# Performance work log

Measured on AMD Instinct MI355X. Metric: run time of the kernel, lower is better.

## Reference

```python
import jax, jax.numpy as jnp
import numpy as np

# Complete K-ary forest: B trees, depth D levels, BFS node numbering per tree.
B, K, D = 64, 4, 6
V, L = 600, 256
N_PER = (K ** D - 1) // (K - 1)   # 1365 nodes per tree
N = B * N_PER                      # 87360 total nodes


def _schedule():
    """Per-(depth, sibling_index) groups, mirroring the torch decode_train loop
    for a complete K-ary forest. Returns list of (d, s, node_idx, parent_idx)."""
    starts = [(K ** d - 1) // (K - 1) for d in range(D)]  # level offsets within a tree
    tree_off = np.arange(B)[:, None] * N_PER
    groups = []
    for d in range(D):
        for s in (range(1) if d == 0 else range(K)):
            if d == 0:
                p = np.arange(1)                      # root
                par = None
            else:
                p = np.arange(K ** (d - 1)) * K + s   # positions with sib_pos == s
                par = (tree_off + starts[d - 1] + (p // K)[None, :]).reshape(-1)
            idx = (tree_off + starts[d] + p[None, :]).reshape(-1)
            groups.append((d, s, jnp.asarray(idx),
                           None if par is None else jnp.asarray(par)))
    return groups

GROUPS = _schedule()


def _lstm(gx, h, c, W_hh, b_ih, b_hh):
    # torch LSTMCell, gate order i, f, g, o; gx = x @ W_ih^T precomputed.
    gates = gx + b_ih + h @ W_hh.T + b_hh
    i, f, g, o = jnp.split(gates, 4, axis=1)
    c_new = jax.nn.sigmoid(f) * c + jax.nn.sigmoid(i) * jnp.tanh(g)
    return jax.nn.sigmoid(o) * jnp.tanh(c_new), c_new


def setup_inputs() -> dict:
    key = jax.random.key(0)
    ks = jax.random.split(key, 20)
    w = lambda k, shape, s=0.05: jax.random.normal(k, shape, dtype=jnp.float32) * s
    return {
        'z': w(ks[0], (B, L), 1.0),
        'features': jax.random.randint(ks[1], (N,), 0, V),
        'W_ih_p': w(ks[2], (4 * L, V)), 'W_hh_p': w(ks[3], (4 * L, L)),
        'b_ih_p': w(ks[4], (4 * L,)), 'b_hh_p': w(ks[5], (4 * L,)),
        'W_ih_s': w(ks[6], (4 * L, V)), 'W_hh_s': w(ks[7], (4 * L, L)),
        'b_ih_s': w(ks[8], (4 * L,)), 'b_hh_s': w(ks[9], (4 * L,)),
        'U_parent': w(ks[10], (L, L)), 'U_sibling': w(ks[11], (L, L)),
        'W_label': w(ks[12], (V, L)), 'b_label': w(ks[13], (V,)),
        'W_depth': w(ks[14], (1, L)), 'b_depth': w(ks[15], (1,)),
        'W_width': w(ks[16], (1, L)), 'b_width': w(ks[17], (1,)),
        'w_off_p': w(ks[18], (1, 1), 1.0), 'w_off_s': w(ks[19], (1, 1), 1.0),
    }


def reference(z, features, W_ih_p, W_hh_p, b_ih_p, b_hh_p,
              W_ih_s, W_hh_s, b_ih_s, b_hh_s, U_parent, U_sibling,
              W_label, b_label, W_depth, b_depth, W_width, b_width,
              w_off_p, w_off_s):
    h_p = jnp.zeros((N, L), jnp.float32)
    c_p = jnp.zeros((N, L), jnp.float32)
    h_s = jnp.zeros((N, L), jnp.float32)
    c_s = jnp.zeros((N, L), jnp.float32)
    pred_labels = jnp.zeros((N, V), jnp.float32)
    pred_is_parent = jnp.zeros((N,), jnp.float32)
    pred_has_sib = jnp.zeros((N,), jnp.float32)

    for d, s, idx, pidx in GROUPS:
        G = idx.shape[0]
        if d == 0:
            h_par, c_par = z, jnp.zeros((B, L), jnp.float32)
        else:
            h_par, c_par = h_p[pidx], c_p[pidx]
        if s == 0:
            h_prev = jnp.zeros((G, L), jnp.float32)
            c_prev = jnp.zeros((G, L), jnp.float32)
        else:
            h_prev, c_prev = h_s[idx - 1], c_s[idx - 1]
        # group-constant teacher flags for a complete K-ary tree
        is_par = 1.0 if d < D - 1 else 0.0
        has_sib = 1.0 if (d > 0 and s < K - 1) else 0.0

        h_pred = jnp.tanh(h_par @ U_parent.T + h_prev @ U_sibling.T)
        logits = h_pred @ W_label.T + b_label
        p_par = jax.nn.sigmoid(h_pred @ W_depth.T + b_depth)[:, 0]
        p_sib = jax.nn.sigmoid(h_pred @ W_width.T + b_width)[:, 0]
        logp = jax.nn.log_softmax(
            logits + w_off_p[0, 0] * is_par + w_off_s[0, 0] * has_sib, axis=1)

        lab = features[idx]
        gx_p = jnp.take(W_ih_p, lab, axis=1).T  # one-hot @ W_ih^T as a gather
        gx_s = jnp.take(W_ih_s, lab, axis=1).T
        hp_new, cp_new = _lstm(gx_p, h_par, c_par, W_hh_p, b_ih_p, b_hh_p)
        hs_new, cs_new = _lstm(gx_s, h_prev, c_prev, W_hh_s, b_ih_s, b_hh_s)

        h_p = h_p.at[idx].set(hp_new)
        c_p = c_p.at[idx].set(cp_new)
        h_s = h_s.at[idx].set(hs_new)
        c_s = c_s.at[idx].set(cs_new)
        pred_labels = pred_labels.at[idx].set(logp)
        pred_is_parent = pred_is_parent.at[idx].set(p_par)
        pred_has_sib = pred_has_sib.at[idx].set(p_sib)

    # pack [N, V+2]: log-softmax labels, p(is_parent), p(has_sibling)
    return jnp.concatenate(
        [pred_labels, pred_is_parent[:, None], pred_has_sib[:, None]], axis=1)
```

## Files before the change

### kernel.cpp

```cpp
#include <hip/hip_runtime.h>


typedef unsigned short u16;
typedef short bf16x8 __attribute__((ext_vector_type(8)));
typedef float f32x4 __attribute__((ext_vector_type(4)));

#define NPER 1365
#define VDIM 600
#define VD2  602

#define MODE_PPA   0
#define MODE_UPROJ 1
#define MODE_ROOT  2

__device__ __forceinline__ float b2f(u16 h) {
  union { unsigned u; float f; } v; v.u = ((unsigned)h) << 16; return v.f;
}
__device__ __forceinline__ u16 f2bf(float f) {
  union { float f; unsigned u; } v; v.f = f;
  unsigned r = v.u + 0x7fff + ((v.u >> 16) & 1);
  return (u16)(r >> 16);
}
__device__ __forceinline__ float fsigm(float x) {
  return __fdividef(1.f, 1.f + __expf(-x));
}
__device__ __forceinline__ float ftanh(float x) {
  float e = __expf(-2.f * fabsf(x));
  float r = __fdividef(1.f - e, 1.f + e);
  return x < 0.f ? -r : r;
}

__device__ __forceinline__ void ladder(int r, int& off, int& pcs, int& start) {
  if (r < 64)        { off = 0;    pcs = 0; start = 1;   }
  else if (r < 320)  { off = 64;   pcs = 2; start = 5;   }
  else if (r < 1344) { off = 320;  pcs = 4; start = 21;  }
  else if (r < 5440) { off = 1344; pcs = 6; start = 85;  }
  else               { off = 5440; pcs = 8; start = 341; }
}

__global__ void k_pack(
    const float* __restrict__ Upar, const float* __restrict__ Whhp,
    const float* __restrict__ Usib, const float* __restrict__ Whhs,
    const float* __restrict__ z, const float* __restrict__ Wihp,
    const float* __restrict__ Wihs, const float* __restrict__ Wlab,
    const float* __restrict__ Wd, const float* __restrict__ Ww,
    const float* __restrict__ blab, const float* __restrict__ bd,
    const float* __restrict__ bw, const float* __restrict__ bihp,
    const float* __restrict__ bhhp, const float* __restrict__ bihs,
    const float* __restrict__ bhhs,
    u16* __restrict__ UPWHHP, u16* __restrict__ USWHHS, u16* __restrict__ ZBF,
    u16* __restrict__ WIHPT, u16* __restrict__ WIHST, u16* __restrict__ WEXT,
    float* __restrict__ BE, float* __restrict__ BP, float* __restrict__ BS) {
  int i = blockIdx.x * 256 + threadIdx.x;
  if (i < 327680) {
    int r = i >> 8, c = i & 255;
    UPWHHP[i] = f2bf(r < 256 ? Upar[(r << 8) | c] : Whhp[((r - 256) << 8) | c]);
    return;
  }
  i -= 327680;
  if (i < 327680) {
    int r = i >> 8, c = i & 255;
    USWHHS[i] = f2bf(r < 256 ? Usib[(r << 8) | c] : Whhs[((r - 256) << 8) | c]);
    return;
  }
  i -= 327680;
  if (i < 16384) { ZBF[i] = f2bf(z[i]); return; }
  i -= 16384;
  if (i < 614400) {
    int r = i >> 10, c = i & 1023;
    WIHPT[i] = f2bf(Wihp[c * VDIM + r]); return;
  }
  i -= 614400;
  if (i < 614400) {
    int r = i >> 10, c = i & 1023;
    WIHST[i] = f2bf(Wihs[c * VDIM + r]); return;
  }
  i -= 614400;
  if (i < VD2 * 256) {
    int r = i >> 8, c = i & 255;
    float v = (r < VDIM) ? Wlab[r * 256 + c] : ((r == VDIM) ? Wd[c] : Ww[c]);
    WEXT[i] = f2bf(v); return;
  }
  i -= VD2 * 256;
  if (i < VD2) { BE[i] = (i < VDIM) ? blab[i] : ((i == VDIM) ? bd[0] : bw[0]); return; }
  i -= VD2;
  if (i < 1024) { BP[i] = bihp[i] + bhhp[i]; return; }
  i -= 1024;
  if (i < 1024) { BS[i] = bihs[i] + bhhs[i]; return; }
}

__device__ __forceinline__ void dev_dual(
    int tile, int nx, const u16* __restrict__ A, const u16* __restrict__ B,
    int M, int mode, u16* __restrict__ ppa, int ppoff,
    float* __restrict__ uproj, u16* __restrict__ gates,
    u16* __restrict__ hpred) {
  static __shared__ __align__(16) u16 As[128 * 40];
  static __shared__ __align__(16) u16 Bs[128 * 40];
  const int m0 = (tile % nx) * 128, n0 = (tile / nx) * 128;
  const int tid = threadIdx.x;
  const int wave = tid >> 6, lane = tid & 63;
  const int quad = lane >> 4, lr = lane & 15;
  const int wm = (wave >> 1) * 64, wn = (wave & 1) * 64;
  const int srow = tid >> 2;
  const int sch = (tid & 3) << 3;

  f32x4 acc[4][4] = {};
  for (int t = 0; t < 8; ++t) {
    const int kk = t * 32;
    bf16x8 a0 = *(const bf16x8*)(A + (size_t)(m0 + srow) * 256 + kk + sch);
    bf16x8 a1 = *(const bf16x8*)(A + (size_t)(m0 + srow + 64) * 256 + kk + sch);
    bf16x8 b0 = *(const bf16x8*)(B + (size_t)(n0 + srow) * 256 + kk + sch);
    bf16x8 b1 = *(const bf16x8*)(B + (size_t)(n0 + srow + 64) * 256 + kk + sch);
    __syncthreads();
    *(bf16x8*)&As[srow * 40 + sch] = a0;
    *(bf16x8*)&As[(srow + 64) * 40 + sch] = a1;
    *(bf16x8*)&Bs[srow * 40 + sch] = b0;
    *(bf16x8*)&Bs[(srow + 64) * 40 + sch] = b1;
    __syncthreads();
    bf16x8 af[4], bfr[4];
#pragma unroll
    for (int tm = 0; tm < 4; ++tm)
      af[tm] = *(const bf16x8*)&As[(wm + tm * 16 + lr) * 40 + quad * 8];
#pragma unroll
    for (int tn = 0; tn < 4; ++tn)
      bfr[tn] = *(const bf16x8*)&Bs[(wn + tn * 16 + lr) * 40 + quad * 8];
#pragma unroll
    for (int tm = 0; tm < 4; ++tm)
#pragma unroll
      for (int tn = 0; tn < 4; ++tn)
        acc[tm][tn] = __builtin_amdgcn_mfma_f32_16x16x32_bf16(
            af[tm], bfr[tn], acc[tm][tn], 0, 0, 0);
  }

  const bool isg = (n0 >= 256);
#pragma unroll
  for (int tn = 0; tn < 4; ++tn) {
    int col = n0 + wn + tn * 16 + lr;
#pragma unroll
    for (int tm = 0; tm < 4; ++tm) {
#pragma unroll
      for (int r = 0; r < 4; ++r) {
        int row = m0 + wm + tm * 16 + quad * 4 + r;
        if (row >= M) continue;
        float v = acc[tm][tn][r];
        if (isg) {
          gates[(size_t)row * 1024 + (col - 256)] = f2bf(v);
        } else if (mode == MODE_PPA) {
          ppa[(size_t)(ppoff + row) * 256 + col] = f2bf(v);
        } else if (mode == MODE_UPROJ) {
          uproj[(size_t)row * 256 + col] = v;
        } else {
          hpred[(size_t)row * NPER * 256 + col] = f2bf(ftanh(v));
        }
      }
    }
  }
}


__device__ __forceinline__ void dev_s0(int r, const u16* __restrict__ wihT,
    const float* __restrict__ bias, const int* __restrict__ feat,
    u16* __restrict__ h, u16* __restrict__ c) {
  int u = threadIdx.x;
  int off, pcs, start; ladder(r, off, pcs, start);
  int lg = r - off;
  int t = lg >> pcs, j = lg & ((1 << pcs) - 1);
  int lab = feat[t * NPER + start + 4 * j];
  const u16* wr = wihT + lab * 1024;
  float gi = b2f(wr[u])       + bias[u];
  float gg = b2f(wr[512 + u]) + bias[512 + u];
  float go = b2f(wr[768 + u]) + bias[768 + u];
  float cn = fsigm(gi) * ftanh(gg);
  float hn = fsigm(go) * ftanh(cn);
  h[(size_t)r * 256 + u] = f2bf(hn);
  c[(size_t)r * 256 + u] = f2bf(cn);
}

__device__ __forceinline__ void dev_lstm_sib(int r, int k,
    const u16* __restrict__ gates, const u16* __restrict__ wihT,
    const float* __restrict__ bias, const u16* __restrict__ c_in,
    const int* __restrict__ feat, u16* __restrict__ h, u16* __restrict__ c) {
  int u = threadIdx.x;
  int off, pcs, start; ladder(r, off, pcs, start);
  int lg = r - off;
  int t = lg >> pcs, j = lg & ((1 << pcs) - 1);
  int lab = feat[t * NPER + start + 4 * j + k];
  const u16* wr = wihT + lab * 1024;
  const u16* gr = gates + (size_t)r * 1024;
  float gi = b2f(wr[u])       + bias[u]       + b2f(gr[u]);
  float gf = b2f(wr[256 + u]) + bias[256 + u] + b2f(gr[256 + u]);
  float gg = b2f(wr[512 + u]) + bias[512 + u] + b2f(gr[512 + u]);
  float go = b2f(wr[768 + u]) + bias[768 + u] + b2f(gr[768 + u]);
  float cv = b2f(c_in[(size_t)r * 256 + u]);
  float cn = fsigm(gf) * cv + fsigm(gi) * ftanh(gg);
  float hn = fsigm(go) * ftanh(cn);
  h[(size_t)r * 256 + u] = f2bf(hn);
  c[(size_t)r * 256 + u] = f2bf(cn);
}

__device__ __forceinline__ void dev_lstm_par(int g,
    const u16* __restrict__ gates, const u16* __restrict__ wihT,
    const float* __restrict__ bias, const u16* __restrict__ c_in,
    const int* __restrict__ feat, u16* __restrict__ h, u16* __restrict__ c,
    int lsbits, int start) {
  int u = threadIdx.x;
  int t = g >> lsbits, p = g & ((1 << lsbits) - 1);
  int pr = lsbits ? ((t << (lsbits - 2)) | (p >> 2)) : g;
  int lab = feat[t * NPER + start + p];
  const u16* wr = wihT + lab * 1024;
  const u16* gr = gates + (size_t)pr * 1024;
  float gi = b2f(wr[u])       + bias[u]       + b2f(gr[u]);
  float gf = b2f(wr[256 + u]) + bias[256 + u] + b2f(gr[256 + u]);
  float gg = b2f(wr[512 + u]) + bias[512 + u] + b2f(gr[512 + u]);
  float go = b2f(wr[768 + u]) + bias[768 + u] + b2f(gr[768 + u]);
  float cv = c_in ? b2f(c_in[(size_t)pr * 256 + u]) : 0.f;
  float cn = fsigm(gf) * cv + fsigm(gi) * ftanh(gg);
  float hn = fsigm(go) * ftanh(cn);
  h[(size_t)g * 256 + u] = f2bf(hn);
  c[(size_t)g * 256 + u] = f2bf(cn);
}

__device__ __forceinline__ void dev_assemble(int r,
    const u16* __restrict__ PPA, const float* __restrict__ U1,
    const float* __restrict__ U2, const float* __restrict__ U3,
    u16* __restrict__ HPRED) {
  int u = threadIdx.x;
  int off, pcs, start; ladder(r, off, pcs, start);
  int lg = r - off;
  int t = lg >> pcs, j = lg & ((1 << pcs) - 1);
  size_t base = ((size_t)(t * NPER + start + 4 * j)) * 256 + u;
  size_t ro = (size_t)r * 256 + u;
  float pp = b2f(PPA[ro]);
  HPRED[base]       = f2bf(ftanh(pp));
  HPRED[base + 256] = f2bf(ftanh(pp + U1[ro]));
  HPRED[base + 512] = f2bf(ftanh(pp + U2[ro]));
  HPRED[base + 768] = f2bf(ftanh(pp + U3[ro]));
}


__global__ __launch_bounds__(256) void k_s0(
    const u16* WIHST, const float* BS, const int* feat, u16* h, u16* c) {
  dev_s0(blockIdx.x, WIHST, BS, feat, h, c);
}

__global__ __launch_bounds__(256) void k_gg(
    int nA,
    const u16* Aa, const u16* Ba, int Ma, int nxa, int modea,
    u16* ppaa, int ppoffa, float* uproja, u16* gatesa, u16* hpreda,
    const u16* Ab, const u16* Bb, int Mb, int nxb, int modeb,
    u16* ppab, int ppoffb, float* uprojb, u16* gatesb, u16* hpredb) {
  int b = blockIdx.x;
  if (b < nA)
    dev_dual(b, nxa, Aa, Ba, Ma, modea, ppaa, ppoffa, uproja, gatesa, hpreda);
  else
    dev_dual(b - nA, nxb, Ab, Bb, Mb, modeb, ppab, ppoffb, uprojb, gatesb,
             hpredb);
}

__global__ __launch_bounds__(256) void k_gemm(
    const u16* A, const u16* B, int M, int nx, int mode,
    u16* ppa, int ppoff, float* uproj, u16* gates, u16* hpred) {
  dev_dual(blockIdx.x, nx, A, B, M, mode, ppa, ppoff, uproj, gates, hpred);
}

__global__ __launch_bounds__(256) void k_ll(
    int nP,
    const u16* gatesP, const u16* WIHPT, const float* BP, const u16* cpin,
    u16* hpout, u16* cpout, int lsbits, int startp,
    int kS, const u16* gatesS, const u16* WIHST, const float* BS,
    const u16* csin, u16* hsout, u16* csout, const int* feat) {
  int b = blockIdx.x;
  if (b < nP)
    dev_lstm_par(b, gatesP, WIHPT, BP, cpin, feat, hpout, cpout, lsbits,
                 startp);
  else
    dev_lstm_sib(b - nP, kS, gatesS, WIHST, BS, csin, feat, hsout, csout);
}

__global__ __launch_bounds__(256) void k_plstm(
    const u16* gatesP, const u16* WIHPT, const float* BP, const u16* cpin,
    const int* feat, u16* hpout, u16* cpout, int lsbits, int start) {
  dev_lstm_par(blockIdx.x, gatesP, WIHPT, BP, cpin, feat, hpout, cpout,
               lsbits, start);
}

__global__ __launch_bounds__(256) void k_plstm_asm(
    const u16* gatesP, const u16* WIHPT, const float* BP, const u16* cpin,
    const int* feat, u16* hpout, u16* cpout,
    const u16* PPA, const float* U1, const float* U2, const float* U3,
    u16* HPRED) {
  int b = blockIdx.x;
  if (b < 16384)
    dev_lstm_par(b, gatesP, WIHPT, BP, cpin, feat, hpout, cpout, 8, 85);
  else
    dev_assemble(b - 16384, PPA, U1, U2, U3, HPRED);
}

__global__ __launch_bounds__(256) void k_assemble(
    const u16* PPA, const float* U1, const float* U2, const float* U3,
    u16* HPRED) {
  dev_assemble(5440 + blockIdx.x, PPA, U1, U2, U3, HPRED);
}

__global__ __launch_bounds__(256, 2) void k_mm_tail(
    const u16* __restrict__ A, const u16* __restrict__ B,
    const float* __restrict__ bias, float* __restrict__ out) {
  __shared__ __align__(16) u16 As[32 * 264];
  __shared__ float smax[32][4], ssum[32][4], slz[32];
  const int m0 = blockIdx.x * 32;
  const int tid = threadIdx.x;
  const int wave = tid >> 6, lane = tid & 63;
  const int quad = lane >> 4, lr = lane & 15;
  const int c0 = wave * 160;

#pragma unroll
  for (int c = 0; c < 4; ++c) {
    int idx = c * 256 + tid;
    int row = idx >> 5, ch = (idx & 31) << 3;
    *(bf16x8*)&As[row * 264 + ch] =
        *(const bf16x8*)(A + (size_t)(m0 + row) * 256 + ch);
  }
  __syncthreads();

  f32x4 acc[2][10] = {};
#pragma unroll
  for (int t = 0; t < 8; ++t) {
    bf16x8 af[2], bfr[10];
#pragma unroll
    for (int tm = 0; tm < 2; ++tm)
      af[tm] = *(const bf16x8*)&As[(tm * 16 + lr) * 264 + t * 32 + quad * 8];
#pragma unroll
    for (int tn = 0; tn < 10; ++tn)
      bfr[tn] = *(const bf16x8*)(B + (size_t)(c0 + tn * 16 + lr) * 256 +
                                 t * 32 + quad * 8);
#pragma unroll
    for (int tm = 0; tm < 2; ++tm)
#pragma unroll
      for (int tn = 0; tn < 10; ++tn)
        acc[tm][tn] = __builtin_amdgcn_mfma_f32_16x16x32_bf16(
            af[tm], bfr[tn], acc[tm][tn], 0, 0, 0);
  }

  float bv[10]; bool val[10];
#pragma unroll
  for (int tn = 0; tn < 10; ++tn) {
    int col = c0 + tn * 16 + lr;
    val[tn] = (col < VDIM);
    bv[tn] = (col < VD2) ? bias[col] : 0.f;
  }

#pragma unroll
  for (int tm = 0; tm < 2; ++tm) {
#pragma unroll
    for (int r = 0; r < 4; ++r) {
      float mx = -1e30f;
#pragma unroll
      for (int tn = 0; tn < 10; ++tn)
        if (val[tn]) mx = fmaxf(mx, acc[tm][tn][r] + bv[tn]);
#pragma unroll
      for (int o = 1; o < 16; o <<= 1) mx = fmaxf(mx, __shfl_xor(mx, o, 64));
      if (lr == 0) smax[tm * 16 + quad * 4 + r][wave] = mx;
    }
  }
  __syncthreads();
#pragma unroll
  for (int tm = 0; tm < 2; ++tm) {
#pragma unroll
    for (int r = 0; r < 4; ++r) {
      int row = tm * 16 + quad * 4 + r;
      float fm = fmaxf(fmaxf(smax[row][0], smax[row][1]),
                       fmaxf(smax[row][2], smax[row][3]));
      float se = 0.f;
#pragma unroll
      for (int tn = 0; tn < 10; ++tn)
        if (val[tn]) se += __expf(acc[tm][tn][r] + bv[tn] - fm);
#pragma unroll
      for (int o = 1; o < 16; o <<= 1) se += __shfl_xor(se, o, 64);
      if (lr == 0) ssum[row][wave] = se;
    }
  }
  __syncthreads();
  if (tid < 32) {
    float fm = fmaxf(fmaxf(smax[tid][0], smax[tid][1]),
                     fmaxf(smax[tid][2], smax[tid][3]));
    slz[tid] = fm + __logf(ssum[tid][0] + ssum[tid][1] +
                           ssum[tid][2] + ssum[tid][3]);
  }
  __syncthreads();

#pragma unroll
  for (int tm = 0; tm < 2; ++tm) {
#pragma unroll
    for (int tn = 0; tn < 10; ++tn) {
      int col = c0 + tn * 16 + lr;
      if (col >= VD2) continue;
#pragma unroll
      for (int r = 0; r < 4; ++r) {
        int row = tm * 16 + quad * 4 + r;
        float v = acc[tm][tn][r] + bv[tn];
        out[(size_t)(m0 + row) * VD2 + col] =
            (col < VDIM) ? (v - slz[row]) : fsigm(v);
      }
    }
  }
}


extern "C" void kernel_launch(void* const* d_in, const int* in_sizes, int n_in,
                              void* d_out, int out_size, void* d_ws, size_t ws_size,
                              hipStream_t stream) {
  const float* z    = (const float*)d_in[0];
  const int*   feat = (const int*)d_in[1];
  const float* Wihp = (const float*)d_in[2];
  const float* Whhp = (const float*)d_in[3];
  const float* bihp = (const float*)d_in[4];
  const float* bhhp = (const float*)d_in[5];
  const float* Wihs = (const float*)d_in[6];
  const float* Whhs = (const float*)d_in[7];
  const float* bihs = (const float*)d_in[8];
  const float* bhhs = (const float*)d_in[9];
  const float* Upar = (const float*)d_in[10];
  const float* Usib = (const float*)d_in[11];
  const float* Wlab = (const float*)d_in[12];
  const float* blab = (const float*)d_in[13];
  const float* Wd   = (const float*)d_in[14];
  const float* bd   = (const float*)d_in[15];
  const float* Ww   = (const float*)d_in[16];
  const float* bw   = (const float*)d_in[17];
  float* out = (float*)d_out;

  char* w = (char*)d_ws;
  auto alloc = [&](size_t bytes) {
    char* p = w; w += (bytes + 255) & ~(size_t)255; return p;
  };
  u16*   UPWHHP = (u16*)alloc((size_t)1280 * 256 * 2);
  u16*   USWHHS = (u16*)alloc((size_t)1280 * 256 * 2);
  u16*   ZBF    = (u16*)alloc((size_t)128 * 256 * 2);
  u16*   WIHPT  = (u16*)alloc((size_t)VDIM * 1024 * 2);
  u16*   WIHST  = (u16*)alloc((size_t)VDIM * 1024 * 2);
  u16*   WEXT   = (u16*)alloc((size_t)640 * 256 * 2);
  float* BE     = (float*)alloc(VD2 * 4);
  float* BP     = (float*)alloc(1024 * 4);
  float* BS     = (float*)alloc(1024 * 4);
  const size_t CR = 21888;
  u16*   HSA[3], *CSA[3];
  for (int k = 0; k < 3; ++k) {
    HSA[k] = (u16*)alloc(CR * 256 * 2);
    CSA[k] = (u16*)alloc(CR * 256 * 2);
  }
  float* UPROJ[3];
  for (int k = 0; k < 3; ++k) UPROJ[k] = (float*)alloc(CR * 256 * 4);
  u16*   PPA   = (u16*)alloc(CR * 256 * 2);
  const size_t SB = (size_t)16384 * 256 * 2;
  u16* HP[2] = {(u16*)alloc(SB), (u16*)alloc(SB)};
  u16* CP[2] = {(u16*)alloc(SB), (u16*)alloc(SB)};
  u16*   GATES  = (u16*)alloc(CR * 1024 * 2);
  u16*   GATESP = (u16*)alloc((size_t)4096 * 1024 * 2);
  u16*   HPRED  = (u16*)alloc((size_t)87424 * 256 * 2);

  k_pack<<<8037, 256, 0, stream>>>(Upar, Whhp, Usib, Whhs, z, Wihp, Wihs,
                                   Wlab, Wd, Ww, blab, bd, bw, bihp, bhhp,
                                   bihs, bhhs, UPWHHP, USWHHS, ZBF, WIHPT,
                                   WIHST, WEXT, BE, BP, BS);
  k_s0<<<21824, 256, 0, stream>>>(WIHST, BS, feat, HSA[0], CSA[0]);
  k_gg<<<10 + 1710, 256, 0, stream>>>(
      10,
      ZBF, UPWHHP, 64, 1, MODE_ROOT, nullptr, 0, nullptr, GATESP, HPRED,
      HSA[0], USWHHS, 21824, 171, MODE_UPROJ, nullptr, 0, UPROJ[0], GATES,
      nullptr);
  k_ll<<<64 + 21824, 256, 0, stream>>>(
      64, GATESP, WIHPT, BP, nullptr, HP[0], CP[0], 0, 0,
      1, GATES, WIHST, BS, CSA[0], HSA[1], CSA[1], feat);
  k_gg<<<10 + 1710, 256, 0, stream>>>(
      10,
      HP[0], UPWHHP, 64, 1, MODE_PPA, PPA, 0, nullptr, GATESP, nullptr,
      HSA[1], USWHHS, 21824, 171, MODE_UPROJ, nullptr, 0, UPROJ[1], GATES,
      nullptr);
  k_ll<<<256 + 21824, 256, 0, stream>>>(
      256, GATESP, WIHPT, BP, CP[0], HP[1], CP[1], 2, 1,
      2, GATES, WIHST, BS, CSA[1], HSA[2], CSA[2], feat);
  k_gg<<<20 + 342, 256, 0, stream>>>(
      20,
      HP[1], UPWHHP, 256, 2, MODE_PPA, PPA, 64, nullptr, GATESP, nullptr,
      HSA[2], USWHHS, 21824, 171, MODE_UPROJ, nullptr, 0, UPROJ[2], nullptr,
      nullptr);
  k_plstm<<<1024, 256, 0, stream>>>(GATESP, WIHPT, BP, CP[1], feat,
                                    HP[0], CP[0], 4, 5);
  k_gemm<<<80, 256, 0, stream>>>(HP[0], UPWHHP, 1024, 8, MODE_PPA,
                                 PPA, 320, nullptr, GATESP, nullptr);
  k_plstm<<<4096, 256, 0, stream>>>(GATESP, WIHPT, BP, CP[0], feat,
                                    HP[1], CP[1], 6, 21);
  k_gemm<<<320, 256, 0, stream>>>(HP[1], UPWHHP, 4096, 32, MODE_PPA,
                                  PPA, 1344, nullptr, GATESP, nullptr);
  k_plstm_asm<<<16384 + 5440, 256, 0, stream>>>(
      GATESP, WIHPT, BP, CP[1], feat, HP[0], CP[0],
      PPA, UPROJ[0], UPROJ[1], UPROJ[2], HPRED);
  k_gemm<<<256, 256, 0, stream>>>(HP[0], UPWHHP, 16384, 128, MODE_PPA,
                                  PPA, 5440, nullptr, nullptr, nullptr);
  k_assemble<<<16384, 256, 0, stream>>>(PPA, UPROJ[0], UPROJ[1], UPROJ[2],
                                        HPRED);
  k_mm_tail<<<2730, 256, 0, stream>>>(HPRED, WEXT, BE, out);

  (void)in_sizes; (void)n_in; (void)out_size; (void)ws_size;
}
```

Before: 620.0 us.

## Fuse sibling LSTM cell into gate GEMM epilogue via interleaved gate layout

Reorders the sibling W_hh and W_ih weights so the four gates of each hidden unit sit in adjacent columns. The GEMM epilogue can then apply the sibling LSTM cell directly, combining the gates with lane shuffles. This removes the GATES intermediate buffer and its write and reread, and shrinks the separate LSTM launch to the parent-only path. The cost is extra epilogue work in the GEMM: per-row label gathers, transcendentals on every output, and only one lane in four doing the writes, which may cut GEMM efficiency.

Measured after the change: 819.0 us. 1.32x slower.

```diff
diff --git a/kernel.cpp b/kernel.cpp
--- a/kernel.cpp
+++ b/kernel.cpp
@@ -12,6 +12,7 @@
 #define MODE_PPA   0
 #define MODE_UPROJ 1
 #define MODE_ROOT  2
+#define MODE_FUSE  3
 
 __device__ __forceinline__ float b2f(u16 h) {
   union { unsigned u; float f; } v; v.u = ((unsigned)h) << 16; return v.f;
@@ -50,7 +51,8 @@
     const float* __restrict__ bhhs,
     u16* __restrict__ UPWHHP, u16* __restrict__ USWHHS, u16* __restrict__ ZBF,
     u16* __restrict__ WIHPT, u16* __restrict__ WIHST, u16* __restrict__ WEXT,
-    float* __restrict__ BE, float* __restrict__ BP, float* __restrict__ BS) {
+    float* __restrict__ BE, float* __restrict__ BP, float* __restrict__ BS,
+    u16* __restrict__ WIHST2, float* __restrict__ BS2) {
   int i = blockIdx.x * 256 + threadIdx.x;
   if (i < 327680) {
     int r = i >> 8, c = i & 255;
@@ -60,7 +62,13 @@
   i -= 327680;
   if (i < 327680) {
     int r = i >> 8, c = i & 255;
-    USWHHS[i] = f2bf(r < 256 ? Usib[(r << 8) | c] : Whhs[((r - 256) << 8) | c]);
+    float v;
+    if (r < 256) v = Usib[(r << 8) | c];
+    else {
+      int cp = r - 256, unit = cp >> 2, gate = cp & 3;
+      v = Whhs[(size_t)(gate * 256 + unit) * 256 + c];
+    }
+    USWHHS[i] = f2bf(v);
     return;
   }
   i -= 327680;
@@ -87,13 +95,28 @@
   if (i < 1024) { BP[i] = bihp[i] + bhhp[i]; return; }
   i -= 1024;
   if (i < 1024) { BS[i] = bihs[i] + bhhs[i]; return; }
+  i -= 1024;
+  if (i < 614400) {
+    int lab = i >> 10, cp = i & 1023;
+    int unit = cp >> 2, gate = cp & 3;
+    WIHST2[i] = f2bf(Wihs[(size_t)(gate * 256 + unit) * VDIM + lab]);
+    return;
+  }
+  i -= 614400;
+  if (i < 1024) {
+    int unit = i >> 2, gate = i & 3;
+    BS2[i] = bihs[gate * 256 + unit] + bhhs[gate * 256 + unit];
+  }
 }
 
 __device__ __forceinline__ void dev_dual(
     int tile, int nx, const u16* __restrict__ A, const u16* __restrict__ B,
     int M, int mode, u16* __restrict__ ppa, int ppoff,
     float* __restrict__ uproj, u16* __restrict__ gates,
-    u16* __restrict__ hpred) {
+    u16* __restrict__ hpred,
+    int kSib, const int* __restrict__ feat, const u16* __restrict__ wih2,
+    const float* __restrict__ bs2, const u16* __restrict__ c_in,
+    u16* __restrict__ h_out, u16* __restrict__ c_out) {
   static __shared__ __align__(16) u16 As[128 * 40];
   static __shared__ __align__(16) u16 Bs[128 * 40];
   const int m0 = (tile % nx) * 128, n0 = (tile / nx) * 128;
@@ -133,6 +156,42 @@
   }
 
   const bool isg = (n0 >= 256);
+
+  if (isg && mode == MODE_FUSE) {
+#pragma unroll
+    for (int tm = 0; tm < 4; ++tm) {
+#pragma unroll
+      for (int r = 0; r < 4; ++r) {
+        int row = m0 + wm + tm * 16 + quad * 4 + r;
+        if (row >= M) continue;
+        int off, pcs, start; ladder(row, off, pcs, start);
+        int lg = row - off;
+        int t = lg >> pcs, j = lg & ((1 << pcs) - 1);
+        int lab = feat[t * NPER + start + 4 * j + kSib];
+        const u16* wr = wih2 + (size_t)lab * 1024;
+#pragma unroll
+        for (int tn = 0; tn < 4; ++tn) {
+          int cp = (n0 - 256) + wn + tn * 16 + lr;
+          float g = acc[tm][tn][r] + bs2[cp] + b2f(wr[cp]);
+          int gid = lr & 3;
+          float a = (gid == 2) ? ftanh(g) : fsigm(g);
+          float x1 = __shfl_xor(a, 1, 64);
+          float x2 = __shfl_xor(a, 2, 64);
+          float x3 = __shfl_xor(x1, 2, 64);
+          if (gid == 0) {
+            int unit = cp >> 2;
+            float cv = b2f(c_in[(size_t)row * 256 + unit]);
+            float cn = x1 * cv + a * x2;
+            float hn = x3 * ftanh(cn);
+            h_out[(size_t)row * 256 + unit] = f2bf(hn);
+            c_out[(size_t)row * 256 + unit] = f2bf(cn);
+          }
+        }
+      }
+    }
+    return;
+  }
+
 #pragma unroll
   for (int tn = 0; tn < 4; ++tn) {
     int col = n0 + wn + tn * 16 + lr;
@@ -147,7 +206,7 @@
           gates[(size_t)row * 1024 + (col - 256)] = f2bf(v);
         } else if (mode == MODE_PPA) {
           ppa[(size_t)(ppoff + row) * 256 + col] = f2bf(v);
-        } else if (mode == MODE_UPROJ) {
+        } else if (mode == MODE_UPROJ || mode == MODE_FUSE) {
           uproj[(size_t)row * 256 + col] = v;
         } else {
           hpred[(size_t)row * NPER * 256 + col] = f2bf(ftanh(v));
@@ -171,28 +230,6 @@
   float gg = b2f(wr[512 + u]) + bias[512 + u];
   float go = b2f(wr[768 + u]) + bias[768 + u];
   float cn = fsigm(gi) * ftanh(gg);
-  float hn = fsigm(go) * ftanh(cn);
-  h[(size_t)r * 256 + u] = f2bf(hn);
-  c[(size_t)r * 256 + u] = f2bf(cn);
-}
-
-__device__ __forceinline__ void dev_lstm_sib(int r, int k,
-    const u16* __restrict__ gates, const u16* __restrict__ wihT,
-    const float* __restrict__ bias, const u16* __restrict__ c_in,
-    const int* __restrict__ feat, u16* __restrict__ h, u16* __restrict__ c) {
-  int u = threadIdx.x;
-  int off, pcs, start; ladder(r, off, pcs, start);
-  int lg = r - off;
-  int t = lg >> pcs, j = lg & ((1 << pcs) - 1);
-  int lab = feat[t * NPER + start + 4 * j + k];
-  const u16* wr = wihT + lab * 1024;
-  const u16* gr = gates + (size_t)r * 1024;
-  float gi = b2f(wr[u])       + bias[u]       + b2f(gr[u]);
-  float gf = b2f(wr[256 + u]) + bias[256 + u] + b2f(gr[256 + u]);
-  float gg = b2f(wr[512 + u]) + bias[512 + u] + b2f(gr[512 + u]);
-  float go = b2f(wr[768 + u]) + bias[768 + u] + b2f(gr[768 + u]);
-  float cv = b2f(c_in[(size_t)r * 256 + u]);
-  float cn = fsigm(gf) * cv + fsigm(gi) * ftanh(gg);
   float hn = fsigm(go) * ftanh(cn);
   h[(size_t)r * 256 + u] = f2bf(hn);
   c[(size_t)r * 256 + u] = f2bf(cn);
@@ -248,33 +285,23 @@
     const u16* Aa, const u16* Ba, int Ma, int nxa, int modea,
     u16* ppaa, int ppoffa, float* uproja, u16* gatesa, u16* hpreda,
     const u16* Ab, const u16* Bb, int Mb, int nxb, int modeb,
-    u16* ppab, int ppoffb, float* uprojb, u16* gatesb, u16* hpredb) {
+    u16* ppab, int ppoffb, float* uprojb, u16* gatesb, u16* hpredb,
+    int kSib, const int* feat, const u16* wih2, const float* bs2,
+    const u16* c_in, u16* h_out, u16* c_out) {
   int b = blockIdx.x;
   if (b < nA)
-    dev_dual(b, nxa, Aa, Ba, Ma, modea, ppaa, ppoffa, uproja, gatesa, hpreda);
+    dev_dual(b, nxa, Aa, Ba, Ma, modea, ppaa, ppoffa, uproja, gatesa, hpreda,
+             0, nullptr, nullptr, nullptr, nullptr, nullptr, nullptr);
   else
     dev_dual(b - nA, nxb, Ab, Bb, Mb, modeb, ppab, ppoffb, uprojb, gatesb,
-             hpredb);
+             hpredb, kSib, feat, wih2, bs2, c_in, h_out, c_out);
 }
 
 __global__ __launch_bounds__(256) void k_gemm(
     const u16* A, const u16* B, int M, int nx, int mode,
     u16* ppa, int ppoff, float* uproj, u16* gates, u16* hpred) {
-  dev_dual(blockIdx.x, nx, A, B, M, mode, ppa, ppoff, uproj, gates, hpred);
-}
-
-__global__ __launch_bounds__(256) void k_ll(
-    int nP,
-    const u16* gatesP, const u16* WIHPT, const float* BP, const u16* cpin,
-    u16* hpout, u16* cpout, int lsbits, int startp,
-    int kS, const u16* gatesS, const u16* WIHST, const float* BS,
-    const u16* csin, u16* hsout, u16* csout, const int* feat) {
-  int b = blockIdx.x;
-  if (b < nP)
-    dev_lstm_par(b, gatesP, WIHPT, BP, cpin, feat, hpout, cpout, lsbits,
-                 startp);
-  else
-    dev_lstm_sib(b - nP, kS, gatesS, WIHST, BS, csin, feat, hsout, csout);
+  dev_dual(blockIdx.x, nx, A, B, M, mode, ppa, ppoff, uproj, gates, hpred,
+           0, nullptr, nullptr, nullptr, nullptr, nullptr, nullptr);
 }
 
 __global__ __launch_bounds__(256) void k_plstm(
@@ -442,6 +469,8 @@
   float* BE     = (float*)alloc(VD2 * 4);
   float* BP     = (float*)alloc(1024 * 4);
   float* BS     = (float*)alloc(1024 * 4);
+  u16*   WIHST2 = (u16*)alloc((size_t)VDIM * 1024 * 2);
+  float* BS2    = (float*)alloc(1024 * 4);
   const size_t CR = 21888;
   u16*   HSA[3], *CSA[3];
   for (int k = 0; k < 3; ++k) {
@@ -454,36 +483,36 @@
   const size_t SB = (size_t)16384 * 256 * 2;
   u16* HP[2] = {(u16*)alloc(SB), (u16*)alloc(SB)};
   u16* CP[2] = {(u16*)alloc(SB), (u16*)alloc(SB)};
-  u16*   GATES  = (u16*)alloc(CR * 1024 * 2);
   u16*   GATESP = (u16*)alloc((size_t)4096 * 1024 * 2);
   u16*   HPRED  = (u16*)alloc((size_t)87424 * 256 * 2);
 
-  k_pack<<<8037, 256, 0, stream>>>(Upar, Whhp, Usib, Whhs, z, Wihp, Wihs,
-                                   Wlab, Wd, Ww, blab, bd, bw, bihp, bhhp,
-                                   bihs, bhhs, UPWHHP, USWHHS, ZBF, WIHPT,
-                                   WIHST, WEXT, BE, BP, BS);
+  k_pack<<<10441, 256, 0, stream>>>(Upar, Whhp, Usib, Whhs, z, Wihp, Wihs,
+                                    Wlab, Wd, Ww, blab, bd, bw, bihp, bhhp,
+                                    bihs, bhhs, UPWHHP, USWHHS, ZBF, WIHPT,
+                                    WIHST, WEXT, BE, BP, BS, WIHST2, BS2);
   k_s0<<<21824, 256, 0, stream>>>(WIHST, BS, feat, HSA[0], CSA[0]);
   k_gg<<<10 + 1710, 256, 0, stream>>>(
       10,
       ZBF, UPWHHP, 64, 1, MODE_ROOT, nullptr, 0, nullptr, GATESP, HPRED,
-      HSA[0], USWHHS, 21824, 171, MODE_UPROJ, nullptr, 0, UPROJ[0], GATES,
-      nullptr);
-  k_ll<<<64 + 21824, 256, 0, stream>>>(
-      64, GATESP, WIHPT, BP, nullptr, HP[0], CP[0], 0, 0,
-      1, GATES, WIHST, BS, CSA[0], HSA[1], CSA[1], feat);
+      HSA[0], USWHHS, 21824, 171, MODE_FUSE, nullptr, 0, UPROJ[0], nullptr,
+      nullptr,
+      1, feat, WIHST2, BS2, CSA[0], HSA[1], CSA[1]);
+  k_plstm<<<64, 256, 0, stream>>>(GATESP, WIHPT, BP, nullptr, feat,
+                                  HP[0], CP[0], 0, 0);
   k_gg<<<10 + 1710, 256, 0, stream>>>(
       10,
       HP[0], UPWHHP, 64, 1, MODE_PPA, PPA, 0, nullptr, GATESP, nullptr,
-      HSA[1], USWHHS, 21824, 171, MODE_UPROJ, nullptr, 0, UPROJ[1], GATES,
-      nullptr);
-  k_ll<<<256 + 21824, 256, 0, stream>>>(
-      256, GATESP, WIHPT, BP, CP[0], HP[1], CP[1], 2, 1,
-      2, GATES, WIHST, BS, CSA[1], HSA[2], CSA[2], feat);
+      HSA[1], USWHHS, 21824, 171, MODE_FUSE, nullptr, 0, UPROJ[1], nullptr,
+      nullptr,
+      2, feat, WIHST2, BS2, CSA[1], HSA[2], CSA[2]);
+  k_plstm<<<256, 256, 0, stream>>>(GATESP, WIHPT, BP, CP[0], feat,
+                                   HP[1], CP[1], 2, 1);
   k_gg<<<20 + 342, 256, 0, stream>>>(
       20,
       HP[1], UPWHHP, 256, 2, MODE_PPA, PPA, 64, nullptr, GATESP, nullptr,
       HSA[2], USWHHS, 21824, 171, MODE_UPROJ, nullptr, 0, UPROJ[2], nullptr,
-      nullptr);
+      nullptr,
+      0, nullptr, nullptr, nullptr, nullptr, nullptr, nullptr);
   k_plstm<<<1024, 256, 0, stream>>>(GATESP, WIHPT, BP, CP[1], feat,
                                     HP[0], CP[0], 4, 5);
   k_gemm<<<80, 256, 0, stream>>>(HP[0], UPWHHP, 1024, 8, MODE_PPA,
```
